# Performance work log

Hardware: AMD Instinct MI355X
Metric: run time of the kernel (lower is better)

The kernel has to match this reference:

```python
import jax, jax.numpy as jnp
import numpy as np

B, S, E, H = 2, 2048, 1024, 16
DH = E // H  # 64
EPS = 1e-5


def layer_norm(x, g, b):
    mu = jnp.mean(x, axis=-1, keepdims=True)
    var = jnp.mean(jnp.square(x - mu), axis=-1, keepdims=True)
    return (x - mu) * jax.lax.rsqrt(var + EPS) * g + b


def setup_inputs() -> dict:
    key = jax.random.key(0)
    ks = jax.random.split(key, 12)
    s = lambda fan_in: 1.0 / np.sqrt(fan_in)
    return {
        "x": jax.random.normal(ks[0], (B, S, E), dtype=jnp.float32),
        "ln1_g": jnp.ones((E,), jnp.float32),
        "ln1_b": jnp.zeros((E,), jnp.float32),
        # per-head projections, batched over head axis: [H, E, DH]
        "Wq": jax.random.uniform(ks[1], (H, E, DH), jnp.float32, -s(E), s(E)),
        "Wk": jax.random.uniform(ks[2], (H, E, DH), jnp.float32, -s(E), s(E)),
        "Wv": jax.random.uniform(ks[3], (H, E, DH), jnp.float32, -s(E), s(E)),
        "Wo": jax.random.uniform(ks[4], (H * DH, E), jnp.float32, -s(H * DH), s(H * DH)),
        "bo": jax.random.uniform(ks[5], (E,), jnp.float32, -s(H * DH), s(H * DH)),
        "ln2_g": jnp.ones((E,), jnp.float32),
        "ln2_b": jnp.zeros((E,), jnp.float32),
        "W1": jax.random.uniform(ks[6], (E, 4 * E), jnp.float32, -s(E), s(E)),
        "b1": jax.random.uniform(ks[7], (4 * E,), jnp.float32, -s(E), s(E)),
        "W2": jax.random.uniform(ks[8], (4 * E, E), jnp.float32, -s(4 * E), s(4 * E)),
        "b2": jax.random.uniform(ks[9], (E,), jnp.float32, -s(4 * E), s(4 * E)),
    }


def reference(x, ln1_g, ln1_b, Wq, Wk, Wv, Wo, bo, ln2_g, ln2_b, W1, b1, W2, b2):
    b, s, e = x.shape
    # --- multi-head attention (pre-LN) ---
    h = layer_norm(x, ln1_g, ln1_b)
    q = jnp.einsum("bse,hed->bhsd", h, Wq)
    k = jnp.einsum("bse,hed->bhsd", h, Wk)
    v = jnp.einsum("bse,hed->bhsd", h, Wv)
    # NOTE: original scales by channel**-0.5 (embed_size), not head_size
    scores = jnp.einsum("bhsd,bhtd->bhst", q, k) * (e ** -0.5)
    causal = jnp.tril(jnp.ones((s, s), dtype=bool))
    scores = jnp.where(causal, scores, -jnp.inf)
    attn = jax.nn.softmax(scores, axis=-1)  # dropout is identity in eval
    out = jnp.einsum("bhst,bhtd->bhsd", attn, v)
    out = out.transpose(0, 2, 1, 3).reshape(b, s, -1)  # concat heads: [B,S,H*DH]
    x = x + out @ Wo + bo
    # --- feed-forward (pre-LN) ---
    h2 = layer_norm(x, ln2_g, ln2_b)
    ff = jax.nn.relu(h2 @ W1 + b1) @ W2 + b2
    return x + ff
```

## Files before the change

kernel.cpp:

```cpp
#include <hip/hip_runtime.h>


typedef __bf16 bf16_t;
typedef __attribute__((ext_vector_type(8))) __bf16 bf16x8;
typedef __attribute__((ext_vector_type(4))) __bf16 bf16x4;
typedef __attribute__((ext_vector_type(4))) float f32x4;

#define B_DIM 2
#define S_DIM 2048
#define E_DIM 1024
#define H_DIM 16
#define DH_DIM 64

#define GLD16(gp, lp) __builtin_amdgcn_global_load_lds( \
    (const __attribute__((address_space(1))) void*)(gp), \
    (__attribute__((address_space(3))) void*)(lp), 16, 0, 0)

#define Q_SCALE 0.0450842120f

__global__ __launch_bounds__(256) void ln_kernel(
    const float* __restrict__ x, const float* __restrict__ g,
    const float* __restrict__ bv, bf16_t* __restrict__ out)
{
  const int row = blockIdx.x;
  const int t = threadIdx.x;
  const float* xr = x + (size_t)row * E_DIM;
  float4 v = *(const float4*)&xr[t * 4];
  float s  = v.x + v.y + v.z + v.w;
  float s2 = v.x*v.x + v.y*v.y + v.z*v.z + v.w*v.w;
#pragma unroll
  for (int m = 1; m < 64; m <<= 1) {
    s  += __shfl_xor(s,  m, 64);
    s2 += __shfl_xor(s2, m, 64);
  }
  __shared__ float red[8];
  const int wid = t >> 6, lane = t & 63;
  if (lane == 0) { red[wid] = s; red[4 + wid] = s2; }
  __syncthreads();
  s  = red[0] + red[1] + red[2] + red[3];
  s2 = red[4] + red[5] + red[6] + red[7];
  const float mu  = s * (1.f / E_DIM);
  const float var = s2 * (1.f / E_DIM) - mu * mu;
  const float rs  = rsqrtf(var + 1e-5f);
  float4 gg = *(const float4*)&g[t * 4];
  float4 bb = *(const float4*)&bv[t * 4];
  bf16x4 o;
  o[0] = (bf16_t)((v.x - mu) * rs * gg.x + bb.x);
  o[1] = (bf16_t)((v.y - mu) * rs * gg.y + bb.y);
  o[2] = (bf16_t)((v.z - mu) * rs * gg.z + bb.z);
  o[3] = (bf16_t)((v.w - mu) * rs * gg.w + bb.w);
  *(bf16x4*)&out[(size_t)row * E_DIM + t * 4] = o;
}

__global__ __launch_bounds__(256) void reduce2_ln(
    const float* __restrict__ p, const float* __restrict__ bo,
    const float* __restrict__ x, const float* __restrict__ g,
    const float* __restrict__ bv, float* __restrict__ xmid, bf16_t* __restrict__ h2)
{
  const int row = blockIdx.x;
  const int t = threadIdx.x;
  const size_t off = (size_t)row * E_DIM + t * 4;
  float4 a  = *(const float4*)&p[off];
  float4 b4 = *(const float4*)&p[(size_t)4096 * E_DIM + off];
  float4 xr = *(const float4*)&x[off];
  float4 bo4 = *(const float4*)&bo[t * 4];
  float4 v;
  v.x = a.x + b4.x + xr.x + bo4.x;
  v.y = a.y + b4.y + xr.y + bo4.y;
  v.z = a.z + b4.z + xr.z + bo4.z;
  v.w = a.w + b4.w + xr.w + bo4.w;
  *(float4*)&xmid[off] = v;
  float s  = v.x + v.y + v.z + v.w;
  float s2 = v.x*v.x + v.y*v.y + v.z*v.z + v.w*v.w;
#pragma unroll
  for (int m = 1; m < 64; m <<= 1) {
    s  += __shfl_xor(s,  m, 64);
    s2 += __shfl_xor(s2, m, 64);
  }
  __shared__ float red[8];
  const int wid = t >> 6, lane = t & 63;
  if (lane == 0) { red[wid] = s; red[4 + wid] = s2; }
  __syncthreads();
  s  = red[0] + red[1] + red[2] + red[3];
  s2 = red[4] + red[5] + red[6] + red[7];
  const float mu  = s * (1.f / E_DIM);
  const float var = s2 * (1.f / E_DIM) - mu * mu;
  const float rs  = rsqrtf(var + 1e-5f);
  float4 gg = *(const float4*)&g[t * 4];
  float4 bb = *(const float4*)&bv[t * 4];
  bf16x4 o;
  o[0] = (bf16_t)((v.x - mu) * rs * gg.x + bb.x);
  o[1] = (bf16_t)((v.y - mu) * rs * gg.y + bb.y);
  o[2] = (bf16_t)((v.z - mu) * rs * gg.z + bb.z);
  o[3] = (bf16_t)((v.w - mu) * rs * gg.w + bb.w);
  *(bf16x4*)&h2[off] = o;
}

__global__ __launch_bounds__(256) void reduce4(
    const bf16_t* __restrict__ p0, const bf16_t* __restrict__ p1,
    const bf16_t* __restrict__ p2, const bf16_t* __restrict__ p3,
    const float* __restrict__ b2, const float* __restrict__ xm,
    float* __restrict__ out)
{
  const int row = blockIdx.x;
  const int t = threadIdx.x;
  const size_t off = (size_t)row * E_DIM + t * 4;
  bf16x4 a0 = *(const bf16x4*)&p0[off];
  bf16x4 a1 = *(const bf16x4*)&p1[off];
  bf16x4 a2 = *(const bf16x4*)&p2[off];
  bf16x4 a3 = *(const bf16x4*)&p3[off];
  float4 xr = *(const float4*)&xm[off];
  float4 bb = *(const float4*)&b2[t * 4];
  float4 o;
  o.x = (float)a0[0] + (float)a1[0] + (float)a2[0] + (float)a3[0] + xr.x + bb.x;
  o.y = (float)a0[1] + (float)a1[1] + (float)a2[1] + (float)a3[1] + xr.y + bb.y;
  o.z = (float)a0[2] + (float)a1[2] + (float)a2[2] + (float)a3[2] + xr.z + bb.z;
  o.w = (float)a0[3] + (float)a1[3] + (float)a2[3] + (float)a3[3] + xr.w + bb.w;
  *(float4*)&out[off] = o;
}

__global__ __launch_bounds__(256) void transpose_cast(
    const float* __restrict__ src, bf16_t* __restrict__ dst, int R, int C)
{
  __shared__ float tile[64][65];
  const int c0 = blockIdx.x * 64, r0 = blockIdx.y * 64;
  const int t = threadIdx.x;
  const int rr = t >> 2;
#pragma unroll
  for (int u = 0; u < 4; u++) {
    const int cc = (t & 3) * 4 + u * 16;
    float4 f = *(const float4*)&src[(size_t)(r0 + rr) * C + c0 + cc];
    tile[rr][cc + 0] = f.x; tile[rr][cc + 1] = f.y;
    tile[rr][cc + 2] = f.z; tile[rr][cc + 3] = f.w;
  }
  __syncthreads();
  const int oc = t >> 2;
#pragma unroll
  for (int u = 0; u < 4; u++) {
    const int orr = (t & 3) * 4 + u * 16;
    bf16x4 w;
    w[0] = (bf16_t)tile[orr + 0][oc];
    w[1] = (bf16_t)tile[orr + 1][oc];
    w[2] = (bf16_t)tile[orr + 2][oc];
    w[3] = (bf16_t)tile[orr + 3][oc];
    *(bf16x4*)&dst[(size_t)(c0 + oc) * R + r0 + orr] = w;
  }
}

__global__ __launch_bounds__(256) void qkv_transpose(
    const float* __restrict__ Wq, const float* __restrict__ Wk,
    const float* __restrict__ Wv, bf16_t* __restrict__ dstT)
{
  const int m = blockIdx.y >> 4, h = blockIdx.y & 15;
  const float* src = (m == 0 ? Wq : (m == 1 ? Wk : Wv)) + (size_t)h * E_DIM * DH_DIM;
  const int e0 = blockIdx.x * 64;
  __shared__ float tile[64][65];
  const int t = threadIdx.x;
  const int rr = t >> 2;
#pragma unroll
  for (int u = 0; u < 4; u++) {
    const int cc = (t & 3) * 4 + u * 16;
    float4 f = *(const float4*)&src[(size_t)(e0 + rr) * DH_DIM + cc];
    tile[rr][cc + 0] = f.x; tile[rr][cc + 1] = f.y;
    tile[rr][cc + 2] = f.z; tile[rr][cc + 3] = f.w;
  }
  __syncthreads();
  const int oc = t >> 2;
  const size_t drow = (size_t)(m * 1024 + h * 64 + oc) * E_DIM;
#pragma unroll
  for (int u = 0; u < 4; u++) {
    const int orr = (t & 3) * 4 + u * 16;
    bf16x4 w;
    w[0] = (bf16_t)tile[orr + 0][oc];
    w[1] = (bf16_t)tile[orr + 1][oc];
    w[2] = (bf16_t)tile[orr + 2][oc];
    w[3] = (bf16_t)tile[orr + 3][oc];
    *(bf16x4*)&dstT[drow + e0 + orr] = w;
  }
}

constexpr int EPI_QKV = 0, EPI_BIAS_RELU = 2, EPI_PART_F32 = 3, EPI_PART_B16 = 4;

template <int EPI>
__global__ __launch_bounds__(512, 2) void gemm256_kernel(
    const bf16_t* __restrict__ A, const bf16_t* __restrict__ Bt,
    int M, int N, int Kst, int Klen,
    const float* __restrict__ bias,
    float* __restrict__ outF, bf16_t* __restrict__ outB,
    bf16_t* __restrict__ qo, bf16_t* __restrict__ ko, bf16_t* __restrict__ vo)
{
  __shared__ bf16_t As[3][256 * 32];
  __shared__ bf16_t Bs[3][256 * 32];

  const int gx = gridDim.x;
  const int nwg = gx * gridDim.y;
  int id = blockIdx.y * gx + blockIdx.x;
  id = (id & 7) * (nwg >> 3) + (id >> 3);
  const int m0 = (id % gx) * 256, n0 = (id / gx) * 256;
  const int sp = blockIdx.z;
  A  += (size_t)sp * Klen;
  Bt += (size_t)sp * Klen;

  const int tid = threadIdx.x, lane = tid & 63, wid = tid >> 6;
  const int wm = wid >> 2, wn = wid & 3;
  const int lr = lane & 15, lg = lane >> 4;

  auto stage = [&](int kt, int buf) {
#pragma unroll
    for (int p = 0; p < 2; p++) {
      const int s = p * 512 + tid;
      const int r = s >> 2;
      const int sl = (s & 3) ^ (r & 3);
      const int ldsoff = (p * 512 + wid * 64) * 8;
      GLD16(A  + (size_t)(m0 + r) * Kst + kt * 32 + sl * 8, &As[buf][ldsoff]);
      GLD16(Bt + (size_t)(n0 + r) * Kst + kt * 32 + sl * 8, &Bs[buf][ldsoff]);
    }
  };

  const f32x4 z4 = {0.f, 0.f, 0.f, 0.f};
  f32x4 acc[8][4];
#pragma unroll
  for (int i = 0; i < 8; i++)
#pragma unroll
    for (int j = 0; j < 4; j++) acc[i][j] = z4;

  const int NT = Klen / 32;
  stage(0, 0);
  stage(1, 1);
  for (int T = 0; T < NT; ++T) {
    const int b = T % 3;
    if (T + 2 < NT) {
      asm volatile("s_waitcnt vmcnt(4)" ::: "memory");
      __builtin_amdgcn_s_barrier();
      stage(T + 2, (T + 2) % 3);
    } else if (T + 1 < NT) {
      asm volatile("s_waitcnt vmcnt(4)" ::: "memory");
      __builtin_amdgcn_s_barrier();
    } else {
      asm volatile("s_waitcnt vmcnt(0)" ::: "memory");
      __builtin_amdgcn_s_barrier();
    }
    __builtin_amdgcn_sched_barrier(0);

    bf16x8 bfr[4];
#pragma unroll
    for (int j = 0; j < 4; j++) {
      const int r = wn * 64 + j * 16 + lr;
      bfr[j] = *(const bf16x8*)&Bs[b][r * 32 + ((lg ^ (lr & 3)) * 8)];
    }
    __builtin_amdgcn_s_setprio(1);
#pragma unroll
    for (int i = 0; i < 8; i++) {
      const int r = wm * 128 + i * 16 + lr;
      bf16x8 af = *(const bf16x8*)&As[b][r * 32 + ((lg ^ (lr & 3)) * 8)];
#pragma unroll
      for (int j = 0; j < 4; j++)
        acc[i][j] = __builtin_amdgcn_mfma_f32_16x16x32_bf16(af, bfr[j], acc[i][j], 0, 0, 0);
    }
    __builtin_amdgcn_s_setprio(0);
  }

#pragma unroll
  for (int i = 0; i < 8; i++) {
#pragma unroll
    for (int j = 0; j < 4; j++) {
#pragma unroll
      for (int r = 0; r < 4; r++) {
        const int m = m0 + wm * 128 + i * 16 + lg * 4 + r;
        const int n = n0 + wn * 64 + j * 16 + lr;
        const float val = acc[i][j][r];
        if constexpr (EPI == EPI_QKV) {
          const int tsel = n >> 10, h = (n >> 6) & 15, d = n & 63;
          const int b_ = m >> 11, s_ = m & 2047;
          const size_t idx = ((size_t)((b_ * H_DIM + h) * S_DIM + s_)) * DH_DIM + d;
          if (tsel == 0)      qo[idx] = (bf16_t)(val * Q_SCALE);
          else if (tsel == 1) ko[idx] = (bf16_t)val;
          else                vo[idx] = (bf16_t)val;
        } else if constexpr (EPI == EPI_BIAS_RELU) {
          const float u = val + bias[n];
          outB[(size_t)m * N + n] = (bf16_t)(u > 0.f ? u : 0.f);
        } else if constexpr (EPI == EPI_PART_F32) {
          outF[(size_t)sp * M * N + (size_t)m * N + n] = val;
        } else {
          bf16_t* o = sp == 0 ? outB : sp == 1 ? qo : sp == 2 ? ko : vo;
          o[(size_t)m * N + n] = (bf16_t)val;
        }
      }
    }
  }
}

__global__ __launch_bounds__(256) void attn_kernel(
    const bf16_t* __restrict__ Q, const bf16_t* __restrict__ K,
    const bf16_t* __restrict__ V, bf16_t* __restrict__ O,
    bf16_t* __restrict__ Opart, float* __restrict__ mpart, float* __restrict__ lpart)
{
  __shared__ bf16_t Ks[2][64 * 64];
  __shared__ bf16_t Vst[2][64 * 64];
  __shared__ bf16_t Ps[4][16 * 64];

  const int nwg = 80 * gridDim.y;
  int id = blockIdx.y * 80 + blockIdx.x;
  id = (id & 7) * (nwg >> 3) + (id >> 3);
  const int bx = id % 80, bh = id / 80;

  int qt, sp, ns;
  if (bx < 8)       { qt = bx;                sp = 0;            ns = 1; }
  else if (bx < 24) { qt = 8 + ((bx - 8) >> 1);  sp = (bx - 8) & 1;  ns = 2; }
  else if (bx < 48) { const int u = bx - 24; const int q3 = u / 3;
                      qt = 16 + q3;           sp = u - q3 * 3;   ns = 3; }
  else              { const int u = bx - 48;  qt = 24 + (u >> 2); sp = u & 3; ns = 4; }
  const int n = qt + 1;
  const int lo = (sp * n) / ns, hi = ((sp + 1) * n) / ns;

  const int q0b = qt * 64;
  const int tid = threadIdx.x;
  const int wid = tid >> 6, lane = tid & 63;
  const int lr = lane & 15, lg = lane >> 4;
  const int q0w = q0b + wid * 16;

  const bf16_t* Qp = Q + (size_t)bh * S_DIM * DH_DIM;
  const bf16_t* Kp = K + (size_t)bh * S_DIM * DH_DIM;
  const bf16_t* Vp = V + (size_t)bh * S_DIM * DH_DIM;

  bf16x8 bq[2];
#pragma unroll
  for (int c = 0; c < 2; c++)
    bq[c] = *(const bf16x8*)&Qp[(size_t)(q0w + lr) * DH_DIM + c * 32 + lg * 8];

  const f32x4 z4 = {0.f, 0.f, 0.f, 0.f};
  f32x4 Ot[4];
#pragma unroll
  for (int dt = 0; dt < 4; dt++) Ot[dt] = z4;
  float mrow = -1e30f, lrow = 0.f;

  const int st = tid >> 3;
  const int s8 = tid & 7;
  const int sbl = lane & 48;
  const int ktr = wid * 8 + (lane >> 3);
  const int ksc = (lane & 7);

  {
    const int t0 = lo * 64;
#pragma unroll
    for (int p = 0; p < 2; p++) {
      const int tr = p * 32 + ktr;
      GLD16(Kp + (size_t)(t0 + tr) * DH_DIM + (ksc ^ (tr & 7)) * 8,
            &Ks[0][(p * 32 + wid * 8) * 64]);
    }
  }
  bf16x8 vc0 = *(const bf16x8*)&Vp[(size_t)(lo * 64 + st) * DH_DIM + s8 * 8];
  bf16x8 vc1 = *(const bf16x8*)&Vp[(size_t)(lo * 64 + 32 + st) * DH_DIM + s8 * 8];
  bf16x8 vn0 = vc0, vn1 = vc1;

  for (int tc = lo; tc < hi; ++tc) {
    const int cur = (tc - lo) & 1;
#pragma unroll
    for (int h2 = 0; h2 < 2; h2++) {
      const bf16x8 vv = h2 ? vc1 : vc0;
      const int t = h2 * 32 + st;
#pragma unroll
      for (int j = 0; j < 8; j++) {
        const int d = s8 * 8 + j;
        const int f = j ^ s8;
        Vst[cur][(d * 128 + ((t * 2) ^ (f << 4))) >> 1] = vv[j];
      }
    }
    __syncthreads();
    if (tc + 1 < hi) {
      const int t1 = (tc + 1) * 64;
#pragma unroll
      for (int p = 0; p < 2; p++) {
        const int tr = p * 32 + ktr;
        GLD16(Kp + (size_t)(t1 + tr) * DH_DIM + (ksc ^ (tr & 7)) * 8,
              &Ks[cur ^ 1][(p * 32 + wid * 8) * 64]);
      }
      vn0 = *(const bf16x8*)&Vp[(size_t)(t1 + st) * DH_DIM + s8 * 8];
      vn1 = *(const bf16x8*)&Vp[(size_t)(t1 + 32 + st) * DH_DIM + s8 * 8];
    }

    const int t0 = tc * 64;
    f32x4 sc[4];
    __builtin_amdgcn_s_setprio(1);
#pragma unroll
    for (int j = 0; j < 4; j++) {
      f32x4 s = z4;
      const int t = j * 16 + lr;
#pragma unroll
      for (int c = 0; c < 2; c++) {
        const int kbyte = t * 128 + (((c * 4 + lg) * 16) ^ ((t & 7) << 4));
        bf16x8 ak = *(const bf16x8*)((const char*)&Ks[cur][0] + kbyte);
        s = __builtin_amdgcn_mfma_f32_16x16x32_bf16(ak, bq[c], s, 0, 0, 0);
      }
      sc[j] = s;
    }
    __builtin_amdgcn_s_setprio(0);
    if (tc == qt) {
#pragma unroll
      for (int j = 0; j < 4; j++)
#pragma unroll
        for (int r = 0; r < 4; r++) {
          const int tg = t0 + j * 16 + lg * 4 + r;
          if (tg > q0w + lr) sc[j][r] = -1e30f;
        }
    }
    float tmax = sc[0][0];
#pragma unroll
    for (int j = 0; j < 4; j++)
#pragma unroll
      for (int r = 0; r < 4; r++) tmax = fmaxf(tmax, sc[j][r]);
    tmax = fmaxf(tmax, __shfl_xor(tmax, 16, 64));
    tmax = fmaxf(tmax, __shfl_xor(tmax, 32, 64));
    const float mnew = fmaxf(mrow, tmax);
    const float fsc = __builtin_exp2f(mrow - mnew);
    mrow = mnew;
    float tsum = 0.f;
#pragma unroll
    for (int j = 0; j < 4; j++)
#pragma unroll
      for (int r = 0; r < 4; r++) {
        const float p = __builtin_exp2f(sc[j][r] - mnew);
        sc[j][r] = p;
        tsum += p;
      }
    tsum += __shfl_xor(tsum, 16, 64);
    tsum += __shfl_xor(tsum, 32, 64);
    lrow = lrow * fsc + tsum;

#pragma unroll
    for (int j = 0; j < 4; j++) {
      bf16x4 w;
#pragma unroll
      for (int r = 0; r < 4; r++) w[r] = (bf16_t)sc[j][r];
      const int pbyte = lr * 128 + ((j * 32 + lg * 8) ^ ((lr & 7) << 4));
      *(bf16x4*)((char*)&Ps[wid][0] + pbyte) = w;
    }
    float fr[4];
#pragma unroll
    for (int r = 0; r < 4; r++) fr[r] = __shfl(fsc, sbl | (lg * 4 + r), 64);
#pragma unroll
    for (int dt = 0; dt < 4; dt++)
#pragma unroll
      for (int r = 0; r < 4; r++) Ot[dt][r] *= fr[r];
    __builtin_amdgcn_s_setprio(1);
#pragma unroll
    for (int c = 0; c < 2; c++) {
      const int abyte = lr * 128 + ((c * 64 + lg * 16) ^ ((lr & 7) << 4));
      bf16x8 pa = *(const bf16x8*)((const char*)&Ps[wid][0] + abyte);
#pragma unroll
      for (int dt = 0; dt < 4; dt++) {
        const int d = dt * 16 + lr;
        const int f = (d & 7) ^ ((d >> 3) & 7);
        const int vbyte = d * 128 + (((c * 4 + lg) * 16) ^ (f << 4));
        bf16x8 bv = *(const bf16x8*)((const char*)&Vst[cur][0] + vbyte);
        Ot[dt] = __builtin_amdgcn_mfma_f32_16x16x32_bf16(pa, bv, Ot[dt], 0, 0, 0);
      }
    }
    __builtin_amdgcn_s_setprio(0);
    vc0 = vn0; vc1 = vn1;
  }

  if (ns == 1) {
    float linv[4];
#pragma unroll
    for (int r = 0; r < 4; r++)
      linv[r] = 1.f / __shfl(lrow, sbl | (lg * 4 + r), 64);
    const int b = bh >> 4, h = bh & 15;
#pragma unroll
    for (int r = 0; r < 4; r++) {
      const int s = q0w + lg * 4 + r;
      const size_t base = ((size_t)(b * S_DIM + s)) * E_DIM + h * DH_DIM;
#pragma unroll
      for (int dt = 0; dt < 4; dt++)
        O[base + dt * 16 + lr] = (bf16_t)(Ot[dt][r] * linv[r]);
    }
  } else {
    const int sbase = (qt < 16) ? 8 + 2 * (qt - 8)
                     : (qt < 24) ? 24 + 3 * (qt - 16) : 48 + 4 * (qt - 24);
    const int slot = bh * 80 + sbase + sp;
    bf16_t* Ob = Opart + (size_t)slot * 64 * 64;
#pragma unroll
    for (int r = 0; r < 4; r++)
#pragma unroll
      for (int dt = 0; dt < 4; dt++)
        Ob[(wid * 16 + lg * 4 + r) * 64 + dt * 16 + lr] = (bf16_t)Ot[dt][r];
    if (lg == 0) {
      mpart[slot * 64 + wid * 16 + lr] = mrow;
      lpart[slot * 64 + wid * 16 + lr] = lrow;
    }
  }
}

__global__ __launch_bounds__(256) void attn_combine(
    const bf16_t* __restrict__ Opart, const float* __restrict__ mpart,
    const float* __restrict__ lpart, bf16_t* __restrict__ O)
{
  const int qt = 8 + blockIdx.x;
  const int bh = blockIdx.y;
  const int ns = (qt < 16) ? 2 : (qt < 24) ? 3 : 4;
  const int sbase = (qt < 16) ? 8 + 2 * (qt - 8)
                   : (qt < 24) ? 24 + 3 * (qt - 16) : 48 + 4 * (qt - 24);
  const int slot0 = bh * 80 + sbase;
  const int tid = threadIdx.x;
  const int q = tid >> 2, d0 = (tid & 3) * 16;

  float M = -1e30f;
  for (int s = 0; s < ns; s++) M = fmaxf(M, mpart[(slot0 + s) * 64 + q]);
  float L = 0.f;
  float acc[16];
#pragma unroll
  for (int j = 0; j < 16; j++) acc[j] = 0.f;
  for (int s = 0; s < ns; s++) {
    const float w = __builtin_exp2f(mpart[(slot0 + s) * 64 + q] - M);
    L += w * lpart[(slot0 + s) * 64 + q];
    const bf16_t* Ob = Opart + ((size_t)(slot0 + s) * 64 + q) * 64 + d0;
    bf16x8 o0 = *(const bf16x8*)Ob;
    bf16x8 o1 = *(const bf16x8*)(Ob + 8);
#pragma unroll
    for (int j = 0; j < 8; j++) { acc[j] += w * (float)o0[j]; acc[8 + j] += w * (float)o1[j]; }
  }
  const float inv = 1.f / L;
  const int b = bh >> 4, h = bh & 15;
  const int srow = qt * 64 + q;
  bf16_t* out = O + ((size_t)(b * S_DIM + srow)) * E_DIM + h * DH_DIM + d0;
  bf16x8 w0, w1;
#pragma unroll
  for (int j = 0; j < 8; j++) { w0[j] = (bf16_t)(acc[j] * inv); w1[j] = (bf16_t)(acc[8 + j] * inv); }
  *(bf16x8*)out = w0;
  *(bf16x8*)(out + 8) = w1;
}

extern "C" void kernel_launch(void* const* d_in, const int* in_sizes, int n_in,
                              void* d_out, int out_size, void* d_ws, size_t ws_size,
                              hipStream_t stream)
{
  const float* x    = (const float*)d_in[0];
  const float* ln1g = (const float*)d_in[1];
  const float* ln1b = (const float*)d_in[2];
  const float* Wq   = (const float*)d_in[3];
  const float* Wk   = (const float*)d_in[4];
  const float* Wv   = (const float*)d_in[5];
  const float* Wo   = (const float*)d_in[6];
  const float* bo   = (const float*)d_in[7];
  const float* ln2g = (const float*)d_in[8];
  const float* ln2b = (const float*)d_in[9];
  const float* W1   = (const float*)d_in[10];
  const float* b1   = (const float*)d_in[11];
  const float* W2   = (const float*)d_in[12];
  const float* b2   = (const float*)d_in[13];

  char* ws = (char*)d_ws;
  bf16_t* WqkvT = (bf16_t*)(ws + 0);
  bf16_t* WoT   = (bf16_t*)(ws + 6291456);
  bf16_t* W1T   = (bf16_t*)(ws + 8388608);
  bf16_t* W2T   = (bf16_t*)(ws + 16777216);
  bf16_t* h1    = (bf16_t*)(ws + 25165824);
  bf16_t* qb    = (bf16_t*)(ws + 33554432);
  bf16_t* kb    = (bf16_t*)(ws + 41943040);
  bf16_t* vb    = (bf16_t*)(ws + 50331648);
  bf16_t* attnb = (bf16_t*)(ws + 58720256);
  float*  xmid  = (float* )(ws + 67108864);
  bf16_t* h2    = (bf16_t*)(ws + 83886080);
  bf16_t* ff1   = (bf16_t*)(ws + 25165824);
  bf16_t* Opart = (bf16_t*)(ws + 67108864);
  float*  mpart = (float* )(ws + 25165824);
  float*  lpart = (float* )(ws + 25821184);
  float*  po    = (float* )(ws + 25165824);
  bf16_t* pf0   = (bf16_t*)(ws + 0);
  bf16_t* pf1   = (bf16_t*)(ws + 8388608);
  bf16_t* pf2   = (bf16_t*)(ws + 58720256);
  bf16_t* pf3   = (bf16_t*)(ws + 83886080);

  qkv_transpose<<<dim3(16, 48), 256, 0, stream>>>(Wq, Wk, Wv, WqkvT);
  transpose_cast<<<dim3(16, 16), 256, 0, stream>>>(Wo, WoT, 1024, 1024);
  transpose_cast<<<dim3(64, 16), 256, 0, stream>>>(W1, W1T, 1024, 4096);
  transpose_cast<<<dim3(16, 64), 256, 0, stream>>>(W2, W2T, 4096, 1024);

  ln_kernel<<<4096, 256, 0, stream>>>(x, ln1g, ln1b, h1);
  gemm256_kernel<EPI_QKV><<<dim3(16, 12, 1), 512, 0, stream>>>(
      h1, WqkvT, 4096, 3072, 1024, 1024, nullptr,
      nullptr, nullptr, qb, kb, vb);
  attn_kernel<<<dim3(80, 32), 256, 0, stream>>>(qb, kb, vb, attnb, Opart, mpart, lpart);
  attn_combine<<<dim3(24, 32), 256, 0, stream>>>(Opart, mpart, lpart, attnb);
  gemm256_kernel<EPI_PART_F32><<<dim3(16, 4, 2), 512, 0, stream>>>(
      attnb, WoT, 4096, 1024, 1024, 512, nullptr,
      po, nullptr, nullptr, nullptr, nullptr);
  reduce2_ln<<<4096, 256, 0, stream>>>(po, bo, x, ln2g, ln2b, xmid, h2);
  gemm256_kernel<EPI_BIAS_RELU><<<dim3(16, 16, 1), 512, 0, stream>>>(
      h2, W1T, 4096, 4096, 1024, 1024, b1,
      nullptr, ff1, nullptr, nullptr, nullptr);
  gemm256_kernel<EPI_PART_B16><<<dim3(16, 4, 4), 512, 0, stream>>>(
      ff1, W2T, 4096, 1024, 4096, 1024, nullptr,
      nullptr, pf0, pf1, pf2, pf3);
  reduce4<<<4096, 256, 0, stream>>>(pf0, pf1, pf2, pf3, b2, xmid, (float*)d_out);

  (void)in_sizes; (void)n_in; (void)out_size; (void)ws_size;
}
```

Baseline: 289.6 us.

## Emit V transposed from QKV GEMM and use 128-tile GEMM for QKV/Wo

```diff
diff --git a/kernel.cpp b/kernel.cpp
--- a/kernel.cpp
+++ b/kernel.cpp
@@ -182,45 +182,44 @@
 constexpr int EPI_QKV = 0, EPI_BIAS_RELU = 2, EPI_PART_F32 = 3, EPI_PART_B16 = 4;
 
 template <int EPI>
-__global__ __launch_bounds__(512, 2) void gemm256_kernel(
+__global__ __launch_bounds__(256) void gemm128_kernel(
     const bf16_t* __restrict__ A, const bf16_t* __restrict__ Bt,
     int M, int N, int Kst, int Klen,
     const float* __restrict__ bias,
     float* __restrict__ outF, bf16_t* __restrict__ outB,
     bf16_t* __restrict__ qo, bf16_t* __restrict__ ko, bf16_t* __restrict__ vo)
 {
-  __shared__ bf16_t As[3][256 * 32];
-  __shared__ bf16_t Bs[3][256 * 32];
-
+  __shared__ bf16_t As[3][128 * 32];
+  __shared__ bf16_t Bs[3][128 * 32];
   const int gx = gridDim.x;
   const int nwg = gx * gridDim.y;
   int id = blockIdx.y * gx + blockIdx.x;
   id = (id & 7) * (nwg >> 3) + (id >> 3);
-  const int m0 = (id % gx) * 256, n0 = (id / gx) * 256;
+  const int m0 = (id % gx) * 128, n0 = (id / gx) * 128;
   const int sp = blockIdx.z;
   A  += (size_t)sp * Klen;
   Bt += (size_t)sp * Klen;
 
   const int tid = threadIdx.x, lane = tid & 63, wid = tid >> 6;
-  const int wm = wid >> 2, wn = wid & 3;
+  const int wr = wid >> 1, wc = wid & 1;
   const int lr = lane & 15, lg = lane >> 4;
 
   auto stage = [&](int kt, int buf) {
 #pragma unroll
     for (int p = 0; p < 2; p++) {
-      const int s = p * 512 + tid;
+      const int s = p * 256 + tid;
       const int r = s >> 2;
       const int sl = (s & 3) ^ (r & 3);
-      const int ldsoff = (p * 512 + wid * 64) * 8;
-      GLD16(A  + (size_t)(m0 + r) * Kst + kt * 32 + sl * 8, &As[buf][ldsoff]);
-      GLD16(Bt + (size_t)(n0 + r) * Kst + kt * 32 + sl * 8, &Bs[buf][ldsoff]);
+      const int lbase = (p * 256 + wid * 64) * 8;
+      GLD16(A  + (size_t)(m0 + r) * Kst + kt * 32 + sl * 8, &As[buf][lbase]);
+      GLD16(Bt + (size_t)(n0 + r) * Kst + kt * 32 + sl * 8, &Bs[buf][lbase]);
     }
   };
 
   const f32x4 z4 = {0.f, 0.f, 0.f, 0.f};
-  f32x4 acc[8][4];
-#pragma unroll
-  for (int i = 0; i < 8; i++)
+  f32x4 acc[4][4];
+#pragma unroll
+  for (int i = 0; i < 4; i++)
 #pragma unroll
     for (int j = 0; j < 4; j++) acc[i][j] = z4;
 
@@ -229,53 +228,50 @@
   stage(1, 1);
   for (int T = 0; T < NT; ++T) {
     const int b = T % 3;
-    if (T + 2 < NT) {
-      asm volatile("s_waitcnt vmcnt(4)" ::: "memory");
-      __builtin_amdgcn_s_barrier();
-      stage(T + 2, (T + 2) % 3);
-    } else if (T + 1 < NT) {
-      asm volatile("s_waitcnt vmcnt(4)" ::: "memory");
-      __builtin_amdgcn_s_barrier();
-    } else {
-      asm volatile("s_waitcnt vmcnt(0)" ::: "memory");
-      __builtin_amdgcn_s_barrier();
-    }
+    if (T + 1 < NT) asm volatile("s_waitcnt vmcnt(4)" ::: "memory");
+    else            asm volatile("s_waitcnt vmcnt(0)" ::: "memory");
+    __builtin_amdgcn_s_barrier();
+    if (T + 2 < NT) stage(T + 2, (T + 2) % 3);
     __builtin_amdgcn_sched_barrier(0);
 
-    bf16x8 bfr[4];
+    bf16x8 af[4], bfr[4];
 #pragma unroll
     for (int j = 0; j < 4; j++) {
-      const int r = wn * 64 + j * 16 + lr;
+      const int r = wc * 64 + j * 16 + lr;
       bfr[j] = *(const bf16x8*)&Bs[b][r * 32 + ((lg ^ (lr & 3)) * 8)];
     }
+#pragma unroll
+    for (int i = 0; i < 4; i++) {
+      const int r = wr * 64 + i * 16 + lr;
+      af[i] = *(const bf16x8*)&As[b][r * 32 + ((lg ^ (lr & 3)) * 8)];
+    }
     __builtin_amdgcn_s_setprio(1);
 #pragma unroll
-    for (int i = 0; i < 8; i++) {
-      const int r = wm * 128 + i * 16 + lr;
-      bf16x8 af = *(const bf16x8*)&As[b][r * 32 + ((lg ^ (lr & 3)) * 8)];
+    for (int i = 0; i < 4; i++)
 #pragma unroll
       for (int j = 0; j < 4; j++)
-        acc[i][j] = __builtin_amdgcn_mfma_f32_16x16x32_bf16(af, bfr[j], acc[i][j], 0, 0, 0);
-    }
+        acc[i][j] = __builtin_amdgcn_mfma_f32_16x16x32_bf16(af[i], bfr[j], acc[i][j], 0, 0, 0);
     __builtin_amdgcn_s_setprio(0);
   }
 
 #pragma unroll
-  for (int i = 0; i < 8; i++) {
+  for (int i = 0; i < 4; i++) {
 #pragma unroll
     for (int j = 0; j < 4; j++) {
 #pragma unroll
       for (int r = 0; r < 4; r++) {
-        const int m = m0 + wm * 128 + i * 16 + lg * 4 + r;
-        const int n = n0 + wn * 64 + j * 16 + lr;
+        const int m = m0 + wr * 64 + i * 16 + lg * 4 + r;
+        const int n = n0 + wc * 64 + j * 16 + lr;
         const float val = acc[i][j][r];
         if constexpr (EPI == EPI_QKV) {
           const int tsel = n >> 10, h = (n >> 6) & 15, d = n & 63;
           const int b_ = m >> 11, s_ = m & 2047;
-          const size_t idx = ((size_t)((b_ * H_DIM + h) * S_DIM + s_)) * DH_DIM + d;
-          if (tsel == 0)      qo[idx] = (bf16_t)(val * Q_SCALE);
-          else if (tsel == 1) ko[idx] = (bf16_t)val;
-          else                vo[idx] = (bf16_t)val;
+          if (tsel == 0)
+            qo[((size_t)((b_ * H_DIM + h) * S_DIM + s_)) * DH_DIM + d] = (bf16_t)(val * Q_SCALE);
+          else if (tsel == 1)
+            ko[((size_t)((b_ * H_DIM + h) * S_DIM + s_)) * DH_DIM + d] = (bf16_t)val;
+          else
+            vo[((size_t)((b_ * H_DIM + h) * DH_DIM + d)) * S_DIM + s_] = (bf16_t)val;
         } else if constexpr (EPI == EPI_BIAS_RELU) {
           const float u = val + bias[n];
           outB[(size_t)m * N + n] = (bf16_t)(u > 0.f ? u : 0.f);
@@ -290,13 +286,107 @@
   }
 }
 
+template <int EPI>
+__global__ __launch_bounds__(512, 2) void gemm256_kernel(
+    const bf16_t* __restrict__ A, const bf16_t* __restrict__ Bt,
+    int M, int N, int Kst, int Klen,
+    const float* __restrict__ bias,
+    float* __restrict__ outF, bf16_t* __restrict__ outB,
+    bf16_t* __restrict__ qo, bf16_t* __restrict__ ko, bf16_t* __restrict__ vo)
+{
+  __shared__ bf16_t As[3][256 * 32];
+  __shared__ bf16_t Bs[3][256 * 32];
+  const int gx = gridDim.x;
+  const int nwg = gx * gridDim.y;
+  int id = blockIdx.y * gx + blockIdx.x;
+  id = (id & 7) * (nwg >> 3) + (id >> 3);
+  const int m0 = (id % gx) * 256, n0 = (id / gx) * 256;
+  const int sp = blockIdx.z;
+  A  += (size_t)sp * Klen;
+  Bt += (size_t)sp * Klen;
+
+  const int tid = threadIdx.x, lane = tid & 63, wid = tid >> 6;
+  const int wm = wid >> 2, wn = wid & 3;
+  const int lr = lane & 15, lg = lane >> 4;
+
+  auto stage = [&](int kt, int buf) {
+#pragma unroll
+    for (int p = 0; p < 2; p++) {
+      const int s = p * 512 + tid;
+      const int r = s >> 2;
+      const int sl = (s & 3) ^ (r & 3);
+      const int ldsoff = (p * 512 + wid * 64) * 8;
+      GLD16(A  + (size_t)(m0 + r) * Kst + kt * 32 + sl * 8, &As[buf][ldsoff]);
+      GLD16(Bt + (size_t)(n0 + r) * Kst + kt * 32 + sl * 8, &Bs[buf][ldsoff]);
+    }
+  };
+
+  const f32x4 z4 = {0.f, 0.f, 0.f, 0.f};
+  f32x4 acc[8][4];
+#pragma unroll
+  for (int i = 0; i < 8; i++)
+#pragma unroll
+    for (int j = 0; j < 4; j++) acc[i][j] = z4;
+
+  const int NT = Klen / 32;
+  stage(0, 0);
+  stage(1, 1);
+  for (int T = 0; T < NT; ++T) {
+    const int b = T % 3;
+    if (T + 1 < NT) asm volatile("s_waitcnt vmcnt(4)" ::: "memory");
+    else            asm volatile("s_waitcnt vmcnt(0)" ::: "memory");
+    __builtin_amdgcn_s_barrier();
+    if (T + 2 < NT) stage(T + 2, (T + 2) % 3);
+    __builtin_amdgcn_sched_barrier(0);
+
+    bf16x8 bfr[4];
+#pragma unroll
+    for (int j = 0; j < 4; j++) {
+      const int r = wn * 64 + j * 16 + lr;
+      bfr[j] = *(const bf16x8*)&Bs[b][r * 32 + ((lg ^ (lr & 3)) * 8)];
+    }
+    __builtin_amdgcn_s_setprio(1);
+#pragma unroll
+    for (int i = 0; i < 8; i++) {
+      const int r = wm * 128 + i * 16 + lr;
+      bf16x8 af = *(const bf16x8*)&As[b][r * 32 + ((lg ^ (lr & 3)) * 8)];
+#pragma unroll
+      for (int j = 0; j < 4; j++)
+        acc[i][j] = __builtin_amdgcn_mfma_f32_16x16x32_bf16(af, bfr[j], acc[i][j], 0, 0, 0);
+    }
+    __builtin_amdgcn_s_setprio(0);
+  }
+
+#pragma unroll
+  for (int i = 0; i < 8; i++) {
+#pragma unroll
+    for (int j = 0; j < 4; j++) {
+#pragma unroll
+      for (int r = 0; r < 4; r++) {
+        const int m = m0 + wm * 128 + i * 16 + lg * 4 + r;
+        const int n = n0 + wn * 64 + j * 16 + lr;
+        const float val = acc[i][j][r];
+        if constexpr (EPI == EPI_BIAS_RELU) {
+          const float u = val + bias[n];
+          outB[(size_t)m * N + n] = (bf16_t)(u > 0.f ? u : 0.f);
+        } else if constexpr (EPI == EPI_PART_F32) {
+          outF[(size_t)sp * M * N + (size_t)m * N + n] = val;
+        } else if constexpr (EPI == EPI_PART_B16) {
+          bf16_t* o = sp == 0 ? outB : sp == 1 ? qo : sp == 2 ? ko : vo;
+          o[(size_t)m * N + n] = (bf16_t)val;
+        }
+      }
+    }
+  }
+}
+
 __global__ __launch_bounds__(256) void attn_kernel(
     const bf16_t* __restrict__ Q, const bf16_t* __restrict__ K,
-    const bf16_t* __restrict__ V, bf16_t* __restrict__ O,
+    const bf16_t* __restrict__ Vt, bf16_t* __restrict__ O,
     bf16_t* __restrict__ Opart, float* __restrict__ mpart, float* __restrict__ lpart)
 {
   __shared__ bf16_t Ks[2][64 * 64];
-  __shared__ bf16_t Vst[2][64 * 64];
+  __shared__ bf16_t Vs[2][64 * 64];
   __shared__ bf16_t Ps[4][16 * 64];
 
   const int nwg = 80 * gridDim.y;
@@ -319,9 +409,9 @@
   const int lr = lane & 15, lg = lane >> 4;
   const int q0w = q0b + wid * 16;
 
-  const bf16_t* Qp = Q + (size_t)bh * S_DIM * DH_DIM;
-  const bf16_t* Kp = K + (size_t)bh * S_DIM * DH_DIM;
-  const bf16_t* Vp = V + (size_t)bh * S_DIM * DH_DIM;
+  const bf16_t* Qp = Q  + (size_t)bh * S_DIM * DH_DIM;
+  const bf16_t* Kp = K  + (size_t)bh * S_DIM * DH_DIM;
+  const bf16_t* Vp = Vt + (size_t)bh * DH_DIM * S_DIM;
 
   bf16x8 bq[2];
 #pragma unroll
@@ -334,50 +424,27 @@
   for (int dt = 0; dt < 4; dt++) Ot[dt] = z4;
   float mrow = -1e30f, lrow = 0.f;
 
-  const int st = tid >> 3;
-  const int s8 = tid & 7;
   const int sbl = lane & 48;
   const int ktr = wid * 8 + (lane >> 3);
-  const int ksc = (lane & 7);
-
-  {
-    const int t0 = lo * 64;
+  const int ksc = lane & 7;
+
+  auto stageKV = [&](int t0, int buf) {
 #pragma unroll
     for (int p = 0; p < 2; p++) {
       const int tr = p * 32 + ktr;
       GLD16(Kp + (size_t)(t0 + tr) * DH_DIM + (ksc ^ (tr & 7)) * 8,
-            &Ks[0][(p * 32 + wid * 8) * 64]);
-    }
-  }
-  bf16x8 vc0 = *(const bf16x8*)&Vp[(size_t)(lo * 64 + st) * DH_DIM + s8 * 8];
-  bf16x8 vc1 = *(const bf16x8*)&Vp[(size_t)(lo * 64 + 32 + st) * DH_DIM + s8 * 8];
-  bf16x8 vn0 = vc0, vn1 = vc1;
+            &Ks[buf][(p * 32 + wid * 8) * 64]);
+      GLD16(Vp + (size_t)tr * S_DIM + t0 + (ksc ^ (tr & 7)) * 8,
+            &Vs[buf][(p * 32 + wid * 8) * 64]);
+    }
+  };
+
+  stageKV(lo * 64, 0);
 
   for (int tc = lo; tc < hi; ++tc) {
     const int cur = (tc - lo) & 1;
-#pragma unroll
-    for (int h2 = 0; h2 < 2; h2++) {
-      const bf16x8 vv = h2 ? vc1 : vc0;
-      const int t = h2 * 32 + st;
-#pragma unroll
-      for (int j = 0; j < 8; j++) {
-        const int d = s8 * 8 + j;
-        const int f = j ^ s8;
-        Vst[cur][(d * 128 + ((t * 2) ^ (f << 4))) >> 1] = vv[j];
-      }
-    }
     __syncthreads();
-    if (tc + 1 < hi) {
-      const int t1 = (tc + 1) * 64;
-#pragma unroll
-      for (int p = 0; p < 2; p++) {
-        const int tr = p * 32 + ktr;
-        GLD16(Kp + (size_t)(t1 + tr) * DH_DIM + (ksc ^ (tr & 7)) * 8,
-              &Ks[cur ^ 1][(p * 32 + wid * 8) * 64]);
-      }
-      vn0 = *(const bf16x8*)&Vp[(size_t)(t1 + st) * DH_DIM + s8 * 8];
-      vn1 = *(const bf16x8*)&Vp[(size_t)(t1 + 32 + st) * DH_DIM + s8 * 8];
-    }
+    if (tc + 1 < hi) stageKV((tc + 1) * 64, cur ^ 1);
 
     const int t0 = tc * 64;
     f32x4 sc[4];
@@ -442,6 +509,7 @@
     for (int dt = 0; dt < 4; dt++)
 #pragma unroll
       for (int r = 0; r < 4; r++) Ot[dt][r] *= fr[r];
+
     __builtin_amdgcn_s_setprio(1);
 #pragma unroll
     for (int c = 0; c < 2; c++) {
@@ -450,14 +518,12 @@
 #pragma unroll
       for (int dt = 0; dt < 4; dt++) {
         const int d = dt * 16 + lr;
-        const int f = (d & 7) ^ ((d >> 3) & 7);
-        const int vbyte = d * 128 + (((c * 4 + lg) * 16) ^ (f << 4));
-        bf16x8 bv = *(const bf16x8*)((const char*)&Vst[cur][0] + vbyte);
+        const int vbyte = d * 128 + (((c * 4 + lg) * 16) ^ ((d & 7) << 4));
+        bf16x8 bv = *(const bf16x8*)((const char*)&Vs[cur][0] + vbyte);
         Ot[dt] = __builtin_amdgcn_mfma_f32_16x16x32_bf16(pa, bv, Ot[dt], 0, 0, 0);
       }
     }
     __builtin_amdgcn_s_setprio(0);
-    vc0 = vn0; vc1 = vn1;
   }
 
   if (ns == 1) {
@@ -577,12 +643,12 @@
   transpose_cast<<<dim3(16, 64), 256, 0, stream>>>(W2, W2T, 4096, 1024);
 
   ln_kernel<<<4096, 256, 0, stream>>>(x, ln1g, ln1b, h1);
-  gemm256_kernel<EPI_QKV><<<dim3(16, 12, 1), 512, 0, stream>>>(
+  gemm128_kernel<EPI_QKV><<<dim3(32, 24, 1), 256, 0, stream>>>(
       h1, WqkvT, 4096, 3072, 1024, 1024, nullptr,
       nullptr, nullptr, qb, kb, vb);
   attn_kernel<<<dim3(80, 32), 256, 0, stream>>>(qb, kb, vb, attnb, Opart, mpart, lpart);
   attn_combine<<<dim3(24, 32), 256, 0, stream>>>(Opart, mpart, lpart, attnb);
-  gemm256_kernel<EPI_PART_F32><<<dim3(16, 4, 2), 512, 0, stream>>>(
+  gemm128_kernel<EPI_PART_F32><<<dim3(32, 8, 2), 256, 0, stream>>>(
       attnb, WoT, 4096, 1024, 1024, 512, nullptr,
       po, nullptr, nullptr, nullptr, nullptr);
   reduce2_ln<<<4096, 256, 0, stream>>>(po, bo, x, ln2g, ln2b, xmid, h2);
```

Measured after the change: 281.0 us. -2.9%, faster.
